# Kernel tuning notes

Measured on AMD Instinct MI355X. Metric: run time of the kernel, lower is better.

Reference implementation:

```python
import jax, jax.numpy as jnp
import numpy as np

NUM_COLUMNS = 16
INPUT_DIM = 1024
NUM_NEURONS = 256
SPARSITY = 0.05
B, S = 4, 2048


def setup_inputs() -> dict:
    key = jax.random.key(0)
    ks = jax.random.split(key, 12)
    D, C, N = INPUT_DIM, NUM_COLUMNS, NUM_NEURONS
    inp = {
        'x': jax.random.normal(ks[0], (B, S, D), dtype=jnp.float32),
        'col_emb': jax.random.normal(ks[1], (C, D), dtype=jnp.float32) * 0.02,
        'gate_w1': jax.random.normal(ks[2], (D, D // 2), dtype=jnp.float32) / np.sqrt(D),
        'gate_b1': jnp.zeros((D // 2,), dtype=jnp.float32),
        'gate_w2': jax.random.normal(ks[3], (D // 2, C), dtype=jnp.float32) / np.sqrt(D // 2),
        'gate_b2': jnp.zeros((C,), dtype=jnp.float32),
        'W_cols': jax.random.normal(ks[4], (C, D, N), dtype=jnp.float32) / np.sqrt(D),
        'b_cols': jnp.zeros((C, N), dtype=jnp.float32),
        'proj_w': jax.random.normal(ks[5], (C * N, D), dtype=jnp.float32) / np.sqrt(C * N),
        'proj_b': jnp.zeros((D,), dtype=jnp.float32),
        'ln_g': jnp.ones((D,), dtype=jnp.float32),
        'ln_b': jnp.zeros((D,), dtype=jnp.float32),
    }
    return inp


def _l2norm(v, axis=-1, eps=1e-12):
    n = jnp.sqrt(jnp.sum(v * v, axis=axis, keepdims=True))
    return v / jnp.maximum(n, eps)


def reference(x, col_emb, gate_w1, gate_b1, gate_w2, gate_b2, W_cols, b_cols,
              proj_w, proj_b, ln_g, ln_b):
    Bq, Sq, D = x.shape
    C = col_emb.shape[0]
    # --- router ---
    similarity = jnp.einsum('bsd,cd->bsc', _l2norm(x), _l2norm(col_emb))
    h = jax.nn.gelu(x @ gate_w1 + gate_b1, approximate=False)
    gate_values = jax.nn.sigmoid(h @ gate_w2 + gate_b2)
    logits = similarity + gate_values  # [B,S,C]
    k = max(1, int(C * SPARSITY))
    _, top_idx = jax.lax.top_k(logits, k)
    mask = jnp.sum(jax.nn.one_hot(top_idx, C, dtype=logits.dtype), axis=-2)  # [B,S,C]
    weights = mask * jax.nn.softmax(logits, axis=-1)
    # --- per-column compute (grouped GEMM), weighted combine ---
    cols = jax.nn.gelu(jnp.einsum('bsd,cdn->bscn', x, W_cols) + b_cols,
                       approximate=False)  # [B,S,C,N]
    cols = cols * weights[..., None]
    combined = cols.reshape(Bq, Sq, -1)  # [B,S,C*N], column-major concat order
    # --- proj + residual + layernorm ---
    y = combined @ proj_w + proj_b + x
    mu = jnp.mean(y, axis=-1, keepdims=True)
    var = jnp.mean((y - mu) ** 2, axis=-1, keepdims=True)
    out = (y - mu) * jax.lax.rsqrt(var + 1e-5) * ln_g + ln_b
    return out
```

## Files before the change

### kernel.cpp

```cpp
#include <hip/hip_runtime.h>
#include <hip/hip_bf16.h>
#include <math.h>

#define D    1024
#define C    16
#define N    256
#define TOK  8192
#define DH   512
#define RT_T 16
#define WLG  160
#define BCAP 20

using bf16x8 = __attribute__((ext_vector_type(8))) short;
using f32x4  = __attribute__((ext_vector_type(4))) float;

__device__ __forceinline__ float gelu_exact(float v) {
    return 0.5f * v * (1.0f + erff(v * 0.70710678118654752440f));
}
__device__ __forceinline__ float sigmoidf_(float z) {
    return 1.0f / (1.0f + expf(-z));
}
__device__ __forceinline__ short f2bf(float f) {
    unsigned u = __float_as_uint(f);
    unsigned r = u + 0x7FFF + ((u >> 16) & 1);
    return (short)(r >> 16);
}
__device__ __forceinline__ float bf2f(short s) {
    return __uint_as_float(((unsigned)(unsigned short)s) << 16);
}

__device__ __forceinline__ void gload16(const void* g, void* l) {
    __builtin_amdgcn_global_load_lds(
        (const __attribute__((address_space(1))) unsigned int*)g,
        (__attribute__((address_space(3))) unsigned int*)l, 16, 0, 0);
}

__device__ __forceinline__ void tconv_body(const float* __restrict__ src0,
        short* __restrict__ dst0, int R, int Cc, int bx, int by, int bz,
        float (*tile)[65], int tid) {
    const size_t bofs = (size_t)bz * R * Cc;
    const float* src = src0 + bofs;
    short* dst = dst0 + bofs;
    const int cBase = bx * 64;
    const int rBase = by * 64;
    const int rr = tid >> 4;
    const int cq = (tid & 15) * 4;
    #pragma unroll
    for (int h = 0; h < 4; ++h) {
        const int r = h * 16 + rr;
        const float4 v = *(const float4*)&src[(size_t)(rBase + r) * Cc + cBase + cq];
        tile[r][cq + 0] = v.x; tile[r][cq + 1] = v.y;
        tile[r][cq + 2] = v.z; tile[r][cq + 3] = v.w;
    }
    __syncthreads();
    #pragma unroll
    for (int h = 0; h < 4; ++h) {
        const int cc = h * 16 + rr;
        short4 o;
        o.x = f2bf(tile[cq + 0][cc]);
        o.y = f2bf(tile[cq + 1][cc]);
        o.z = f2bf(tile[cq + 2][cc]);
        o.w = f2bf(tile[cq + 3][cc]);
        *(short4*)&dst[(size_t)(cBase + cc) * R + rBase + cq] = o;
    }
}

__global__ __launch_bounds__(256) void prep_all_kernel(
        const float* __restrict__ x, const float* __restrict__ col_emb,
        const float* __restrict__ gate_w1, const float* __restrict__ W_cols,
        const float* __restrict__ proj_w,
        short* __restrict__ xb, short* __restrict__ w1T,
        short* __restrict__ WcT, short* __restrict__ pwT,
        float* __restrict__ cnorm) {
    __shared__ float tile[64][65];
    const int b = blockIdx.x;
    const int tid = threadIdx.x;
    if (b == 0) {
        const int c = tid >> 4, l = tid & 15;
        float acc = 0.f;
        for (int j = 0; j < 64; ++j) {
            float v = col_emb[c * D + l + 16 * j];
            acc += v * v;
        }
        for (int off = 8; off; off >>= 1) acc += __shfl_xor(acc, off, 16);
        if (l == 0) cnorm[c] = fmaxf(sqrtf(acc), 1e-12f);
    } else if (b < 2049) {
        const int base = (b - 1) * 1024;
        #pragma unroll
        for (int h = 0; h < 4; ++h) {
            const int i = base + h * 256 + tid;
            const float4 v = ((const float4*)x)[i];
            short4 o;
            o.x = f2bf(v.x); o.y = f2bf(v.y); o.z = f2bf(v.z); o.w = f2bf(v.w);
            ((short4*)xb)[i] = o;
        }
    } else if (b < 2177) {
        const int idx = b - 2049;
        tconv_body(gate_w1, w1T, D, DH, idx & 7, idx >> 3, 0, tile, tid);
    } else if (b < 3201) {
        const int idx = b - 2177;
        tconv_body(W_cols, WcT, D, N, idx & 3, (idx >> 2) & 15, idx >> 6, tile, tid);
    } else {
        const int idx = b - 3201;
        tconv_body(proj_w, pwT, N, D, idx & 15, (idx >> 4) & 3, idx >> 6, tile, tid);
    }
}

__global__ __launch_bounds__(256) void gate_mfma_kernel(
        const short* __restrict__ Ag, const short* __restrict__ BTg,
        const float* __restrict__ bias, short* __restrict__ outb) {
    __shared__ short AB[2][(128 + 64) * 64];
    const int tid = threadIdx.x;
    const int lane = tid & 63;
    const int wave = tid >> 6;
    const int wr = wave >> 1, wc = wave & 1;

    const size_t m0 = (size_t)blockIdx.x * 128;
    const int n0 = blockIdx.y * 64;

    const int rl = lane >> 3;
    const int bl = (lane & 7) * 16;
    const char* gAh[4];
    #pragma unroll
    for (int h = 0; h < 4; ++h) {
        const int r = wave * 32 + h * 8 + rl;
        gAh[h] = (const char*)Ag + (m0 + r) * (size_t)(D * 2) + (bl ^ ((r & 7) << 4));
    }
    const char* gBh[2];
    #pragma unroll
    for (int h = 0; h < 2; ++h) {
        const int r = wave * 16 + h * 8 + rl;
        gBh[h] = (const char*)BTg + (size_t)(n0 + r) * (D * 2) + (bl ^ ((r & 7) << 4));
    }

    const int swz = ((lane & 7)) << 4;
    const int kb0 = (lane >> 4) * 16;

    f32x4 acc[4][2] = {};
    {
        char* Ab = (char*)AB[0];
        char* Bb = (char*)AB[0] + 16384;
        #pragma unroll
        for (int h = 0; h < 4; ++h) gload16(gAh[h], Ab + (wave * 32 + h * 8) * 128);
        #pragma unroll
        for (int h = 0; h < 2; ++h) gload16(gBh[h], Bb + (wave * 16 + h * 8) * 128);
    }
    __syncthreads();
    for (int kk = 0; kk < D / 64; ++kk) {
        const int cur = kk & 1;
        if (kk + 1 < D / 64) {
            const int ko = (kk + 1) * 128;
            char* Ab = (char*)AB[cur ^ 1];
            char* Bb = (char*)AB[cur ^ 1] + 16384;
            #pragma unroll
            for (int h = 0; h < 4; ++h) gload16(gAh[h] + ko, Ab + (wave * 32 + h * 8) * 128);
            #pragma unroll
            for (int h = 0; h < 2; ++h) gload16(gBh[h] + ko, Bb + (wave * 16 + h * 8) * 128);
        }
        const char* As = (const char*)AB[cur];
        const char* Bs = As + 16384;
        #pragma unroll
        for (int ks = 0; ks < 2; ++ks) {
            const int kb = kb0 + ks * 64;
            bf16x8 aF[4], bF[2];
            #pragma unroll
            for (int i = 0; i < 4; ++i)
                aF[i] = *(const bf16x8*)(As + (wr * 64 + i * 16 + (lane & 15)) * 128
                                         + (kb ^ swz));
            #pragma unroll
            for (int j = 0; j < 2; ++j)
                bF[j] = *(const bf16x8*)(Bs + (wc * 32 + j * 16 + (lane & 15)) * 128
                                         + (kb ^ swz));
            #pragma unroll
            for (int i = 0; i < 4; ++i)
                #pragma unroll
                for (int j = 0; j < 2; ++j)
                    acc[i][j] = __builtin_amdgcn_mfma_f32_16x16x32_bf16(
                                    aF[i], bF[j], acc[i][j], 0, 0, 0);
        }
        __syncthreads();
    }
    const int crow = (lane >> 4) * 4;
    const int ccol = lane & 15;
    #pragma unroll
    for (int i = 0; i < 4; ++i)
        #pragma unroll
        for (int j = 0; j < 2; ++j) {
            const int n = n0 + wc * 32 + j * 16 + ccol;
            const float bb = bias[n];
            #pragma unroll
            for (int r = 0; r < 4; ++r) {
                const int m = (int)m0 + wr * 64 + i * 16 + crow + r;
                outb[(size_t)m * DH + n] = f2bf(gelu_exact(acc[i][j][r] + bb));
            }
        }
}

__global__ __launch_bounds__(256) void col1_kernel(
        const short* __restrict__ Ag, const short* __restrict__ BTg,
        const float* __restrict__ bias,
        const int* __restrict__ order, const float* __restrict__ wgt,
        const int* __restrict__ wl, short* __restrict__ outb) {
    __shared__ short AB[2][2][64 * 64];
    __shared__ int   tokl[64];
    __shared__ float wgl[64];

    const int e = wl[blockIdx.x];
    if (e < 0) return;
    const int col  = e >> 24;
    const int nt   = (e >> 16) & 0xFF;
    const int base = e & 0xFFFF;

    const int tid = threadIdx.x;
    const int lane = tid & 63;
    const int wave = tid >> 6;
    const int wr = wave >> 1, wc = wave & 1;
    const int n0 = blockIdx.y * 64;

    if (tid < 64) {
        const int i = tid < nt ? tid : nt - 1;
        const int t = order[base + i];
        tokl[tid] = t;
        wgl[tid] = wgt[t];
    }
    __syncthreads();

    const int r0 = wave * 16 + (lane >> 3);
    const int r1 = r0 + 8;
    const int bl = (lane & 7) * 16;
    const int b0 = bl ^ ((r0 & 7) << 4);
    const int b1 = bl ^ ((r1 & 7) << 4);
    const char* gA0 = (const char*)Ag + (size_t)tokl[r0] * (D * 2) + b0;
    const char* gA1 = (const char*)Ag + (size_t)tokl[r1] * (D * 2) + b1;
    const size_t bbase = ((size_t)col * N + n0) * (D * 2);
    const char* gB0 = (const char*)BTg + bbase + (size_t)r0 * (D * 2) + b0;
    const char* gB1 = (const char*)BTg + bbase + (size_t)r1 * (D * 2) + b1;
    const int ldsWo = wave * 2048;

    const int mrow = wr * 32 + (lane & 15);
    const int nrow = wc * 32 + (lane & 15);
    const int kb0 = (lane >> 4) * 16;
    const int swm = (mrow & 7) << 4;
    const int swn = (nrow & 7) << 4;

    f32x4 acc[2][2] = {};
    {
        char* lA = (char*)AB[0][0] + ldsWo;
        char* lB = (char*)AB[0][1] + ldsWo;
        gload16(gA0, lA); gload16(gA1, lA + 1024);
        gload16(gB0, lB); gload16(gB1, lB + 1024);
    }
    __syncthreads();
    for (int kk = 0; kk < D / 64; ++kk) {
        const int cur = kk & 1;
        if (kk + 1 < D / 64) {
            const int ko = (kk + 1) * 128;
            char* lA = (char*)AB[cur ^ 1][0] + ldsWo;
            char* lB = (char*)AB[cur ^ 1][1] + ldsWo;
            gload16(gA0 + ko, lA); gload16(gA1 + ko, lA + 1024);
            gload16(gB0 + ko, lB); gload16(gB1 + ko, lB + 1024);
        }
        const char* As = (const char*)AB[cur][0];
        const char* Bs = (const char*)AB[cur][1];
        #pragma unroll
        for (int ks = 0; ks < 2; ++ks) {
            const int kb = kb0 + ks * 64;
            bf16x8 aF[2], bF[2];
            #pragma unroll
            for (int i = 0; i < 2; ++i)
                aF[i] = *(const bf16x8*)(As + (mrow + i * 16) * 128 + (kb ^ swm));
            #pragma unroll
            for (int j = 0; j < 2; ++j)
                bF[j] = *(const bf16x8*)(Bs + (nrow + j * 16) * 128 + (kb ^ swn));
            #pragma unroll
            for (int i = 0; i < 2; ++i)
                #pragma unroll
                for (int j = 0; j < 2; ++j)
                    acc[i][j] = __builtin_amdgcn_mfma_f32_16x16x32_bf16(
                                    aF[i], bF[j], acc[i][j], 0, 0, 0);
        }
        __syncthreads();
    }

    const int crow = (lane >> 4) * 4;
    const int ccol = lane & 15;
    #pragma unroll
    for (int i = 0; i < 2; ++i)
        #pragma unroll
        for (int j = 0; j < 2; ++j) {
            const int n = n0 + wc * 32 + j * 16 + ccol;
            const float bb = bias[col * N + n];
            #pragma unroll
            for (int r = 0; r < 4; ++r) {
                const int il = wr * 32 + i * 16 + crow + r;
                if (il < nt) {
                    const float v = gelu_exact(acc[i][j][r] + bb) * wgl[il];
                    outb[(size_t)(base + il) * N + n] = f2bf(v);
                }
            }
        }
}

__global__ __launch_bounds__(256) void proj_kernel(
        const short* __restrict__ Ag, const short* __restrict__ BTg,
        const float* __restrict__ bias, const float* __restrict__ x,
        const int* __restrict__ order, const int* __restrict__ wl,
        float* __restrict__ outf) {
    __shared__ short Bs2[2][64 * 64];
    __shared__ int   tokl[64];

    const int e = wl[blockIdx.x];
    if (e < 0) return;
    const int col  = e >> 24;
    const int nt   = (e >> 16) & 0xFF;
    const int base = e & 0xFFFF;

    const int tid = threadIdx.x;
    const int lane = tid & 63;
    const int wave = tid >> 6;
    const int wr = wave >> 1, wc = wave & 1;
    const int n0 = blockIdx.y * 64;

    bf16x8 aF[4][2][2];
    #pragma unroll
    for (int i = 0; i < 2; ++i) {
        const int m = wr * 32 + i * 16 + (lane & 15);
        const int s = base + min(m, nt - 1);
        const char* ga = (const char*)Ag + (size_t)s * (N * 2) + (lane >> 4) * 16;
        #pragma unroll
        for (int kk = 0; kk < 4; ++kk)
            #pragma unroll
            for (int ks = 0; ks < 2; ++ks)
                aF[kk][i][ks] = *(const bf16x8*)(ga + kk * 128 + ks * 64);
    }

    if (tid < 64) {
        const int i = tid < nt ? tid : nt - 1;
        tokl[tid] = order[base + i];
    }

    const int r0 = wave * 16 + (lane >> 3);
    const int r1 = r0 + 8;
    const int bl = (lane & 7) * 16;
    const int b0 = bl ^ ((r0 & 7) << 4);
    const int b1 = bl ^ ((r1 & 7) << 4);
    const size_t bbase = ((size_t)col * D + n0) * (N * 2);
    const char* gB0 = (const char*)BTg + bbase + (size_t)r0 * (N * 2) + b0;
    const char* gB1 = (const char*)BTg + bbase + (size_t)r1 * (N * 2) + b1;
    const int ldsWo = wave * 2048;

    const int nrow = wc * 32 + (lane & 15);
    const int kb0 = (lane >> 4) * 16;
    const int swn = (nrow & 7) << 4;

    f32x4 acc[2][2] = {};
    {
        char* lB = (char*)Bs2[0] + ldsWo;
        gload16(gB0, lB); gload16(gB1, lB + 1024);
    }
    __syncthreads();
    #pragma unroll
    for (int kk = 0; kk < 4; ++kk) {
        const int cur = kk & 1;
        if (kk + 1 < 4) {
            const int ko = (kk + 1) * 128;
            char* lB = (char*)Bs2[cur ^ 1] + ldsWo;
            gload16(gB0 + ko, lB); gload16(gB1 + ko, lB + 1024);
        }
        const char* Bs = (const char*)Bs2[cur];
        #pragma unroll
        for (int ks = 0; ks < 2; ++ks) {
            const int kb = kb0 + ks * 64;
            bf16x8 bF[2];
            #pragma unroll
            for (int j = 0; j < 2; ++j)
                bF[j] = *(const bf16x8*)(Bs + (nrow + j * 16) * 128 + (kb ^ swn));
            #pragma unroll
            for (int i = 0; i < 2; ++i)
                #pragma unroll
                for (int j = 0; j < 2; ++j)
                    acc[i][j] = __builtin_amdgcn_mfma_f32_16x16x32_bf16(
                                    aF[kk][i][ks], bF[j], acc[i][j], 0, 0, 0);
        }
        __syncthreads();
    }

    const int crow = (lane >> 4) * 4;
    const int ccol = lane & 15;
    #pragma unroll
    for (int i = 0; i < 2; ++i)
        #pragma unroll
        for (int j = 0; j < 2; ++j) {
            const int dcol = n0 + wc * 32 + j * 16 + ccol;
            const float bb = bias[dcol];
            #pragma unroll
            for (int r = 0; r < 4; ++r) {
                const int il = wr * 32 + i * 16 + crow + r;
                if (il < nt) {
                    const size_t ofs = (size_t)tokl[il] * D + dcol;
                    outf[ofs] = acc[i][j][r] + bb + x[ofs];
                }
            }
        }
}

__global__ __launch_bounds__(256) void route_kernel(
        const float* __restrict__ x, const short* __restrict__ Hb,
        const float* __restrict__ col_emb, const float* __restrict__ cnorm,
        const float* __restrict__ w2, const float* __restrict__ b2,
        int* __restrict__ idx, float* __restrict__ wgt) {
    __shared__ float P[256][33];
    __shared__ float Q[8][33];
    __shared__ float SSW[4];
    __shared__ float FL[RT_T][34];
    const int tid = threadIdx.x;
    const int lane = tid & 63;
    const int t0 = blockIdx.x * RT_T;
    const int swz = (tid & 7) << 2;

    float4 ce[C];
    #pragma unroll
    for (int c = 0; c < C; ++c)
        ce[c] = *(const float4*)&col_emb[c * D + tid * 4];
    float w2r[2][C];
    #pragma unroll
    for (int r2 = 0; r2 < 2; ++r2)
        #pragma unroll
        for (int cq = 0; cq < 4; ++cq) {
            const float4 v = *(const float4*)&w2[(tid * 2 + r2) * C + cq * 4];
            w2r[r2][cq * 4 + 0] = v.x; w2r[r2][cq * 4 + 1] = v.y;
            w2r[r2][cq * 4 + 2] = v.z; w2r[r2][cq * 4 + 3] = v.w;
        }

    for (int ti = 0; ti < RT_T; ++ti) {
        const int t = t0 + ti;
        const float4 xv = *(const float4*)&x[(size_t)t * D + tid * 4];
        const unsigned hu = *(const unsigned*)&Hb[(size_t)t * DH + tid * 2];
        const float h0 = bf2f((short)(hu & 0xffff));
        const float h1 = bf2f((short)(hu >> 16));
        float pv[32];
        #pragma unroll
        for (int c = 0; c < C; ++c)
            pv[c] = xv.x * ce[c].x + xv.y * ce[c].y + xv.z * ce[c].z + xv.w * ce[c].w;
        #pragma unroll
        for (int c = 0; c < C; ++c)
            pv[C + c] = h0 * w2r[0][c] + h1 * w2r[1][c];
        float ssp = xv.x * xv.x + xv.y * xv.y + xv.z * xv.z + xv.w * xv.w;
        #pragma unroll
        for (int off = 32; off; off >>= 1) ssp += __shfl_xor(ssp, off);
        if (lane == 0) SSW[tid >> 6] = ssp;
        #pragma unroll
        for (int c = 0; c < 32; ++c)
            P[tid][c ^ swz] = pv[c];
        __syncthreads();
        {
            const int v = tid & 31, jj = tid >> 5;
            float s = 0.f;
            #pragma unroll
            for (int k = 0; k < 32; ++k) {
                const int row = jj * 32 + k;
                s += P[row][v ^ ((row & 7) << 2)];
            }
            Q[jj][v] = s;
        }
        __syncthreads();
        if (tid < 32) {
            float f = 0.f;
            #pragma unroll
            for (int j2 = 0; j2 < 8; ++j2) f += Q[j2][tid];
            FL[ti][tid] = f;
        } else if (tid == 32) {
            FL[ti][32] = SSW[0] + SSW[1] + SSW[2] + SSW[3];
        }
        __syncthreads();
    }

    if (tid < RT_T) {
        const int t = t0 + tid;
        const float xn = fmaxf(sqrtf(FL[tid][32]), 1e-12f);
        float logit[C];
        #pragma unroll
        for (int c = 0; c < C; ++c)
            logit[c] = FL[tid][c] / (xn * cnorm[c])
                     + sigmoidf_(FL[tid][C + c] + b2[c]);
        float mx = logit[0]; int am = 0;
        #pragma unroll
        for (int c = 1; c < C; ++c)
            if (logit[c] > mx) { mx = logit[c]; am = c; }
        float se = 0.f;
        #pragma unroll
        for (int c = 0; c < C; ++c) se += expf(logit[c] - mx);
        idx[t] = am;
        wgt[t] = 1.f / se;
    }
}

__global__ __launch_bounds__(256) void hist_kernel(const int* __restrict__ idx,
        int* __restrict__ cursor, int* __restrict__ wl) {
    __shared__ int h[C];
    const int tid = threadIdx.x;
    const int lane = tid & 63;
    const int wave = tid >> 6;
    if (tid < C) h[tid] = 0;
    for (int i = tid; i < WLG; i += 256) wl[i] = -1;
    __syncthreads();
    int cnt = 0;
    for (int t0 = wave * 64; t0 < TOK; t0 += 256) {
        const int c = idx[t0 + lane];
        #pragma unroll
        for (int cc = 0; cc < C; ++cc) {
            const unsigned long long m = __ballot(c == cc);
            if (lane == cc) cnt += (int)__popcll(m);
        }
    }
    if (lane < C) atomicAdd(&h[lane], cnt);
    __syncthreads();
    if (tid == 0) {
        int s = 0;
        int slots[8] = {0, 0, 0, 0, 0, 0, 0, 0};
        for (int c = 0; c < C; ++c) {
            cursor[c] = s;
            for (int st = 0; st < h[c]; st += 64) {
                const int ntg = min(64, h[c] - st);
                int b = c & 7;
                while (slots[b] >= BCAP) b = (b + 1) & 7;
                wl[slots[b] * 8 + b] = (c << 24) | (ntg << 16) | (s + st);
                slots[b]++;
            }
            s += h[c];
        }
    }
}

__global__ __launch_bounds__(256) void scatter_kernel(const int* __restrict__ idx,
        int* __restrict__ cursor, int* __restrict__ order) {
    __shared__ int lh[C];
    __shared__ int lbase[C];
    const int tid = threadIdx.x;
    const int t = blockIdx.x * 256 + tid;
    if (tid < C) lh[tid] = 0;
    __syncthreads();
    const int c = idx[t];
    const int p = atomicAdd(&lh[c], 1);
    __syncthreads();
    if (tid < C) lbase[tid] = atomicAdd(&cursor[tid], lh[tid]);
    __syncthreads();
    order[lbase[c] + p] = t;
}

__global__ __launch_bounds__(256) void ln_kernel(float* __restrict__ out,
        const float* __restrict__ g, const float* __restrict__ b) {
    __shared__ float wr_[4], wr2[4];
    const int t = blockIdx.x, tid = threadIdx.x;
    const float4 v = *(const float4*)&out[(size_t)t * D + tid * 4];
    float s = v.x + v.y + v.z + v.w;
    float s2 = v.x * v.x + v.y * v.y + v.z * v.z + v.w * v.w;
    for (int off = 32; off; off >>= 1) { s += __shfl_xor(s, off); s2 += __shfl_xor(s2, off); }
    if ((tid & 63) == 0) { wr_[tid >> 6] = s; wr2[tid >> 6] = s2; }
    __syncthreads();
    const float sum = wr_[0] + wr_[1] + wr_[2] + wr_[3];
    const float sum2 = wr2[0] + wr2[1] + wr2[2] + wr2[3];
    const float mu = sum * (1.f / D);
    const float var = sum2 * (1.f / D) - mu * mu;
    const float inv = rsqrtf(var + 1e-5f);
    const float4 g4 = *(const float4*)&g[tid * 4];
    const float4 b4 = *(const float4*)&b[tid * 4];
    float4 o;
    o.x = (v.x - mu) * inv * g4.x + b4.x;
    o.y = (v.y - mu) * inv * g4.y + b4.y;
    o.z = (v.z - mu) * inv * g4.z + b4.z;
    o.w = (v.w - mu) * inv * g4.w + b4.w;
    *(float4*)&out[(size_t)t * D + tid * 4] = o;
}

extern "C" void kernel_launch(void* const* d_in, const int* in_sizes, int n_in,
                              void* d_out, int out_size, void* d_ws, size_t ws_size,
                              hipStream_t stream) {
    const float* x       = (const float*)d_in[0];
    const float* col_emb = (const float*)d_in[1];
    const float* gate_w1 = (const float*)d_in[2];
    const float* gate_b1 = (const float*)d_in[3];
    const float* gate_w2 = (const float*)d_in[4];
    const float* gate_b2 = (const float*)d_in[5];
    const float* W_cols  = (const float*)d_in[6];
    const float* b_cols  = (const float*)d_in[7];
    const float* proj_w  = (const float*)d_in[8];
    const float* proj_b  = (const float*)d_in[9];
    const float* ln_g    = (const float*)d_in[10];
    const float* ln_b    = (const float*)d_in[11];
    float* out = (float*)d_out;

    char* w = (char*)d_ws;
    short* xb    = (short*)w;  w += (size_t)TOK * D * 2;
    short* Hb    = (short*)w;  w += (size_t)TOK * DH * 2;
    short* actb  = (short*)w;  w += (size_t)TOK * N * 2 + 65536;
    short* w1T   = (short*)w;  w += (size_t)DH * D * 2;
    short* WcT   = (short*)w;  w += (size_t)C * N * D * 2;
    short* pwT   = (short*)w;  w += (size_t)C * D * N * 2;
    float* wgt   = (float*)w;  w += TOK * 4;
    float* cnorm = (float*)w;  w += 64;
    int*   idx   = (int*)w;    w += TOK * 4;
    int*   order = (int*)w;    w += TOK * 4;
    int*   cursor= (int*)w;    w += 64;
    int*   wl    = (int*)w;    w += WLG * 4;

    hipLaunchKernelGGL(prep_all_kernel, dim3(4225), dim3(256), 0, stream,
                       x, col_emb, gate_w1, W_cols, proj_w,
                       xb, w1T, WcT, pwT, cnorm);
    hipLaunchKernelGGL(gate_mfma_kernel, dim3(TOK / 128, DH / 64), dim3(256), 0, stream,
                       xb, w1T, gate_b1, Hb);
    hipLaunchKernelGGL(route_kernel, dim3(TOK / RT_T), dim3(256), 0, stream,
                       x, Hb, col_emb, cnorm, gate_w2, gate_b2, idx, wgt);
    hipLaunchKernelGGL(hist_kernel, dim3(1), dim3(256), 0, stream, idx, cursor, wl);
    hipLaunchKernelGGL(scatter_kernel, dim3(TOK / 256), dim3(256), 0, stream,
                       idx, cursor, order);
    hipLaunchKernelGGL(col1_kernel, dim3(WLG, N / 64), dim3(256), 0, stream,
                       xb, WcT, b_cols, order, wgt, wl, actb);
    hipLaunchKernelGGL(proj_kernel, dim3(WLG, D / 64), dim3(256), 0, stream,
                       actb, pwT, proj_b, x, order, wl, out);
    hipLaunchKernelGGL(ln_kernel, dim3(TOK), dim3(256), 0, stream, out, ln_g, ln_b);
}
```

Baseline: 177.4 us.

## Write proj output in sorted order and move residual/scatter into layernorm

The projection kernel now writes contiguous rows in the sorted-token order to a new fp32 buffer, replacing the scattered writes and the scattered residual read of x. The residual add and the un-permute scatter move into the layernorm kernel, which gathers one row of x per block and writes the output row. The A operand of the proj GEMM is now staged through double-buffered, swizzled LDS together with B, instead of being preloaded into registers. This adds a 32 MB intermediate buffer and one more full read and write of it.

```diff
diff --git a/kernel.cpp b/kernel.cpp
--- a/kernel.cpp
+++ b/kernel.cpp
@@ -303,12 +303,9 @@
 
 __global__ __launch_bounds__(256) void proj_kernel(
         const short* __restrict__ Ag, const short* __restrict__ BTg,
-        const float* __restrict__ bias, const float* __restrict__ x,
-        const int* __restrict__ order, const int* __restrict__ wl,
-        float* __restrict__ outf) {
-    __shared__ short Bs2[2][64 * 64];
-    __shared__ int   tokl[64];
-
+        const float* __restrict__ bias, const int* __restrict__ wl,
+        float* __restrict__ ybuf) {
+    __shared__ short AB[2][2][64 * 64];
     const int e = wl[blockIdx.x];
     if (e < 0) return;
     const int col  = e >> 24;
@@ -321,57 +318,53 @@
     const int wr = wave >> 1, wc = wave & 1;
     const int n0 = blockIdx.y * 64;
 
-    bf16x8 aF[4][2][2];
-    #pragma unroll
-    for (int i = 0; i < 2; ++i) {
-        const int m = wr * 32 + i * 16 + (lane & 15);
-        const int s = base + min(m, nt - 1);
-        const char* ga = (const char*)Ag + (size_t)s * (N * 2) + (lane >> 4) * 16;
-        #pragma unroll
-        for (int kk = 0; kk < 4; ++kk)
-            #pragma unroll
-            for (int ks = 0; ks < 2; ++ks)
-                aF[kk][i][ks] = *(const bf16x8*)(ga + kk * 128 + ks * 64);
-    }
-
-    if (tid < 64) {
-        const int i = tid < nt ? tid : nt - 1;
-        tokl[tid] = order[base + i];
-    }
-
     const int r0 = wave * 16 + (lane >> 3);
     const int r1 = r0 + 8;
     const int bl = (lane & 7) * 16;
     const int b0 = bl ^ ((r0 & 7) << 4);
     const int b1 = bl ^ ((r1 & 7) << 4);
+    const int s0 = base + min(r0, nt - 1);
+    const int s1 = base + min(r1, nt - 1);
+    const char* gA0 = (const char*)Ag + (size_t)s0 * (N * 2) + b0;
+    const char* gA1 = (const char*)Ag + (size_t)s1 * (N * 2) + b1;
     const size_t bbase = ((size_t)col * D + n0) * (N * 2);
     const char* gB0 = (const char*)BTg + bbase + (size_t)r0 * (N * 2) + b0;
     const char* gB1 = (const char*)BTg + bbase + (size_t)r1 * (N * 2) + b1;
     const int ldsWo = wave * 2048;
 
+    const int mrow = wr * 32 + (lane & 15);
     const int nrow = wc * 32 + (lane & 15);
     const int kb0 = (lane >> 4) * 16;
+    const int swm = (mrow & 7) << 4;
     const int swn = (nrow & 7) << 4;
 
     f32x4 acc[2][2] = {};
     {
-        char* lB = (char*)Bs2[0] + ldsWo;
+        char* lA = (char*)AB[0][0] + ldsWo;
+        char* lB = (char*)AB[0][1] + ldsWo;
+        gload16(gA0, lA); gload16(gA1, lA + 1024);
         gload16(gB0, lB); gload16(gB1, lB + 1024);
     }
     __syncthreads();
     #pragma unroll
-    for (int kk = 0; kk < 4; ++kk) {
+    for (int kk = 0; kk < N / 64; ++kk) {
         const int cur = kk & 1;
-        if (kk + 1 < 4) {
+        if (kk + 1 < N / 64) {
             const int ko = (kk + 1) * 128;
-            char* lB = (char*)Bs2[cur ^ 1] + ldsWo;
+            char* lA = (char*)AB[cur ^ 1][0] + ldsWo;
+            char* lB = (char*)AB[cur ^ 1][1] + ldsWo;
+            gload16(gA0 + ko, lA); gload16(gA1 + ko, lA + 1024);
             gload16(gB0 + ko, lB); gload16(gB1 + ko, lB + 1024);
         }
-        const char* Bs = (const char*)Bs2[cur];
+        const char* As = (const char*)AB[cur][0];
+        const char* Bs = (const char*)AB[cur][1];
         #pragma unroll
         for (int ks = 0; ks < 2; ++ks) {
             const int kb = kb0 + ks * 64;
-            bf16x8 bF[2];
+            bf16x8 aF[2], bF[2];
+            #pragma unroll
+            for (int i = 0; i < 2; ++i)
+                aF[i] = *(const bf16x8*)(As + (mrow + i * 16) * 128 + (kb ^ swm));
             #pragma unroll
             for (int j = 0; j < 2; ++j)
                 bF[j] = *(const bf16x8*)(Bs + (nrow + j * 16) * 128 + (kb ^ swn));
@@ -380,7 +373,7 @@
                 #pragma unroll
                 for (int j = 0; j < 2; ++j)
                     acc[i][j] = __builtin_amdgcn_mfma_f32_16x16x32_bf16(
-                                    aF[kk][i][ks], bF[j], acc[i][j], 0, 0, 0);
+                                    aF[i], bF[j], acc[i][j], 0, 0, 0);
         }
         __syncthreads();
     }
@@ -396,10 +389,8 @@
             #pragma unroll
             for (int r = 0; r < 4; ++r) {
                 const int il = wr * 32 + i * 16 + crow + r;
-                if (il < nt) {
-                    const size_t ofs = (size_t)tokl[il] * D + dcol;
-                    outf[ofs] = acc[i][j][r] + bb + x[ofs];
-                }
+                if (il < nt)
+                    ybuf[(size_t)(base + il) * D + dcol] = acc[i][j][r] + bb;
             }
         }
 }
@@ -548,11 +539,17 @@
     order[lbase[c] + p] = t;
 }
 
-__global__ __launch_bounds__(256) void ln_kernel(float* __restrict__ out,
-        const float* __restrict__ g, const float* __restrict__ b) {
+__global__ __launch_bounds__(256) void ln_kernel(const float* __restrict__ ybuf,
+        const float* __restrict__ x, const int* __restrict__ order,
+        const float* __restrict__ g, const float* __restrict__ b,
+        float* __restrict__ out) {
     __shared__ float wr_[4], wr2[4];
-    const int t = blockIdx.x, tid = threadIdx.x;
-    const float4 v = *(const float4*)&out[(size_t)t * D + tid * 4];
+    const int s0 = blockIdx.x, tid = threadIdx.x;
+    const int row = order[s0];
+    const float4 yv = *(const float4*)&ybuf[(size_t)s0 * D + tid * 4];
+    const float4 xv = *(const float4*)&x[(size_t)row * D + tid * 4];
+    float4 v;
+    v.x = yv.x + xv.x; v.y = yv.y + xv.y; v.z = yv.z + xv.z; v.w = yv.w + xv.w;
     float s = v.x + v.y + v.z + v.w;
     float s2 = v.x * v.x + v.y * v.y + v.z * v.z + v.w * v.w;
     for (int off = 32; off; off >>= 1) { s += __shfl_xor(s, off); s2 += __shfl_xor(s2, off); }
@@ -570,7 +567,7 @@
     o.y = (v.y - mu) * inv * g4.y + b4.y;
     o.z = (v.z - mu) * inv * g4.z + b4.z;
     o.w = (v.w - mu) * inv * g4.w + b4.w;
-    *(float4*)&out[(size_t)t * D + tid * 4] = o;
+    *(float4*)&out[(size_t)row * D + tid * 4] = o;
 }
 
 extern "C" void kernel_launch(void* const* d_in, const int* in_sizes, int n_in,
@@ -597,6 +594,7 @@
     short* w1T   = (short*)w;  w += (size_t)DH * D * 2;
     short* WcT   = (short*)w;  w += (size_t)C * N * D * 2;
     short* pwT   = (short*)w;  w += (size_t)C * D * N * 2;
+    float* ybuf  = (float*)w;  w += (size_t)TOK * D * 4;
     float* wgt   = (float*)w;  w += TOK * 4;
     float* cnorm = (float*)w;  w += 64;
     int*   idx   = (int*)w;    w += TOK * 4;
@@ -617,6 +615,7 @@
     hipLaunchKernelGGL(col1_kernel, dim3(WLG, N / 64), dim3(256), 0, stream,
                        xb, WcT, b_cols, order, wgt, wl, actb);
     hipLaunchKernelGGL(proj_kernel, dim3(WLG, D / 64), dim3(256), 0, stream,
-                       actb, pwT, proj_b, x, order, wl, out);
-    hipLaunchKernelGGL(ln_kernel, dim3(TOK), dim3(256), 0, stream, out, ln_g, ln_b);
-}
+                       actb, pwT, proj_b, wl, ybuf);
+    hipLaunchKernelGGL(ln_kernel, dim3(TOK), dim3(256), 0, stream,
+                       ybuf, x, order, ln_g, ln_b, out);
+}
```

New measurement: 151.9 us. 14.4% less time.
